# Kernel optimization log

Measured on AMD Instinct MI355X. Metric: run time of the kernel, lower is better.

Reference implementation:

```python
import jax, jax.numpy as jnp
import numpy as np

D_MODEL, N_STATE, L_MAX, BATCH = 256, 64, 2048, 16

def _to_c(x):
    return jax.lax.complex(x[..., 0], x[..., 1])

def setup_inputs() -> dict:
    key = jax.random.key(0)
    k_u, k_ct_r, k_ct_i, k_step = jax.random.split(key, 4)
    n, d = N_STATE, D_MODEL
    # --- HiPPO DPLR init (numpy, matches torch hippo_dplr) ---
    P = np.sqrt(1.0 + 2.0 * np.arange(1, n + 1, dtype=np.float64))
    A = np.tril(np.outer(P, P)) - np.diag(np.arange(1, n + 1, dtype=np.float64))
    A = -A
    p = 0.5 * np.sqrt(2.0 * np.arange(1, n + 1, dtype=np.float64) + 1.0)
    Ap = (A + np.outer(p, p)).astype(np.complex64)
    lam, V = np.linalg.eig(Ap)
    p_rot = V.conj().T @ p.astype(np.complex64)
    p_ri = np.stack([p_rot.real, p_rot.imag], -1).astype(np.float32)          # (n,2)
    lambda_ri = np.stack([lam.real, lam.imag], -1).astype(np.float32)         # (n,2)
    # --- B init: sqrt(2k+1), repeated over channels, zero imag ---
    B_r = np.sqrt(2.0 * np.arange(1, n + 1) + 1.0).astype(np.float32)
    B_ri = np.stack([np.tile(B_r, (d, 1)), np.zeros((d, n), np.float32)], -1) # (d,n,2)
    # --- Ct: xavier-normal complex ---
    std = float(np.sqrt(2.0 / (d + n)))
    Ct_r = jax.random.normal(k_ct_r, (d, n), jnp.float32) * (std / np.sqrt(2.0))
    Ct_i = jax.random.normal(k_ct_i, (d, n), jnp.float32) * (std / np.sqrt(2.0))
    Ct_ri = jnp.stack([Ct_r, Ct_i], -1)                                        # (d,n,2)
    Dp = jnp.ones((1, 1, d), jnp.float32)
    log_step = jax.random.uniform(k_step, (d,), jnp.float32) * (
        np.log(0.1) - np.log(0.001)) + np.log(0.001)
    u = jax.random.normal(k_u, (BATCH, L_MAX, d), jnp.float32)
    return {"u": u, "p_ri": jnp.asarray(p_ri), "lambda_ri": jnp.asarray(lambda_ri),
            "B_ri": jnp.asarray(B_ri), "Ct_ri": Ct_ri, "Dp": Dp, "log_step": log_step}

def reference(u, p_ri, lambda_ri, B_ri, Ct_ri, Dp, log_step):
    p = _to_c(p_ri)          # (n,)
    lam = _to_c(lambda_ri)   # (n,)
    B = _to_c(B_ri)          # (d,n)
    Ct = _to_c(Ct_ri)        # (d,n)
    L = u.shape[1]
    omega = jnp.exp(2j * jnp.pi * jnp.arange(L) / L).astype(jnp.complex64)  # (L,)
    step = jnp.exp(log_step)                                               # (d,)
    g = (2.0 / step)[:, None] * ((1.0 - omega) / (1.0 + omega))[None, :]   # (d,L)
    c = 2.0 / (1.0 + omega)                                                # (L,)
    inv = 1.0 / (g[:, :, None] - lam[None, None, :])                       # (d,L,n)
    k00 = jnp.einsum('dn,dln->dl', Ct.conj() * B, inv)
    k01 = jnp.einsum('dn,dln->dl', Ct.conj() * p[None, :], inv)
    k10 = jnp.einsum('dn,dln->dl', p.conj()[None, :] * B, inv)
    k11 = jnp.einsum('n,dln->dl', p.conj() * p, inv)
    at_roots = c[None, :] * (k00 - k01 * k10 / (1.0 + k11))                # (d,L)
    out = jnp.fft.ifft(at_roots, n=L, axis=-1)
    order = jnp.concatenate([jnp.zeros((1,), jnp.int32), jnp.arange(L - 1, 0, -1)])
    K = out[:, order].real[None]                                           # (1,d,L)
    # causal FFT convolution
    ud = jnp.fft.rfft(jnp.pad(u, ((0, 0), (0, L), (0, 0))), axis=1)        # (B,L+1,d)
    Kd = jnp.fft.rfft(jnp.pad(K, ((0, 0), (0, 0), (0, L))), axis=-1)       # (1,d,L+1)
    y = jnp.fft.irfft(jnp.transpose(ud, (0, 2, 1)) * Kd, axis=-1)[..., :L]
    y = jnp.transpose(y, (0, 2, 1)).astype(u.dtype)                        # (B,L,d)
    return y + Dp * u
```

## Files before the change

### kernel.cpp

```cpp
#include <hip/hip_runtime.h>
#include <math.h>

#define LLEN   2048
#define NFFT   4096
#define DMODEL 256
#define NSTATE 64
#define NBATCH 16
#define PI_F   3.14159265358979323846f

#define PADIDX(a) ((a) + ((a) >> 4))
#define LDSN  (NFFT + (NFFT >> 4))
#define LDSN2 (LLEN + (LLEN >> 4))
#define KSTRIDE 2056

__device__ inline float frcp(float x) { return __builtin_amdgcn_rcpf(x); }

#define RADIX4(ar0,ai0,ar1,ai1,ar2,ai2,ar3,ai3,S) do {                      \
    float s0r=(ar0)+(ar2), s0i=(ai0)+(ai2);                                 \
    float s1r=(ar0)-(ar2), s1i=(ai0)-(ai2);                                 \
    float s2r=(ar1)+(ar3), s2i=(ai1)+(ai3);                                 \
    float s3r=(ar1)-(ar3), s3i=(ai1)-(ai3);                                 \
    (ar0)=s0r+s2r; (ai0)=s0i+s2i;                                           \
    (ar2)=s0r-s2r; (ai2)=s0i-s2i;                                           \
    (ar1)=s1r-(S)*s3i; (ai1)=s1i+(S)*s3r;                                   \
    (ar3)=s1r+(S)*s3i; (ai3)=s1i-(S)*s3r;                                   \
} while (0)

template<int SIGN>
__device__ inline void dft16(float xr[16], float xi[16]) {
    const float S = (float)SIGN;
    const float C1 = 0.9238795325112867f, S1 = 0.3826834323650898f;
    const float C2 = 0.7071067811865476f;
    RADIX4(xr[0],xi[0], xr[4],xi[4], xr[8],xi[8],  xr[12],xi[12], S);
    RADIX4(xr[1],xi[1], xr[5],xi[5], xr[9],xi[9],  xr[13],xi[13], S);
    RADIX4(xr[2],xi[2], xr[6],xi[6], xr[10],xi[10],xr[14],xi[14], S);
    RADIX4(xr[3],xi[3], xr[7],xi[7], xr[11],xi[11],xr[15],xi[15], S);
#define TW(idx, wr_, wi_) { float tr = xr[idx]*(wr_) - xi[idx]*(wi_);       \
    xi[idx] = xr[idx]*(wi_) + xi[idx]*(wr_); xr[idx] = tr; }
    TW(5,  C1,  S*S1);
    TW(6,  C2,  S*C2);
    TW(7,  S1,  S*C1);
    TW(9,  C2,  S*C2);
    TW(10, 0.f, S);
    TW(11, -C2, S*C2);
    TW(13, S1,  S*C1);
    TW(14, -C2, S*C2);
    TW(15, -C1, -S*S1);
#undef TW
    RADIX4(xr[0],xi[0],  xr[1],xi[1],  xr[2],xi[2],  xr[3],xi[3],  S);
    RADIX4(xr[4],xi[4],  xr[5],xi[5],  xr[6],xi[6],  xr[7],xi[7],  S);
    RADIX4(xr[8],xi[8],  xr[9],xi[9],  xr[10],xi[10],xr[11],xi[11],S);
    RADIX4(xr[12],xi[12],xr[13],xi[13],xr[14],xi[14],xr[15],xi[15],S);
}

template<int SIGN>
__device__ inline void dft8(float xr[8], float xi[8]) {
    const float S = (float)SIGN;
    const float C2 = 0.7071067811865476f;
    RADIX4(xr[0],xi[0], xr[2],xi[2], xr[4],xi[4], xr[6],xi[6], S);
    RADIX4(xr[1],xi[1], xr[3],xi[3], xr[5],xi[5], xr[7],xi[7], S);
    { float tr = xr[3]*C2 - xi[3]*(S*C2); xi[3] = xr[3]*(S*C2) + xi[3]*C2; xr[3] = tr; }
    { float tr = -S*xi[5]; xi[5] = S*xr[5]; xr[5] = tr; }
    { float tr = xr[7]*(-C2) - xi[7]*(S*C2); xi[7] = xr[7]*(S*C2) + xi[7]*(-C2); xr[7] = tr; }
    float br[8], bi[8];
#pragma unroll
    for (int k = 0; k < 4; ++k) {
        br[k]   = xr[2*k] + xr[2*k+1]; bi[k]   = xi[2*k] + xi[2*k+1];
        br[k+4] = xr[2*k] - xr[2*k+1]; bi[k+4] = xi[2*k] - xi[2*k+1];
    }
#pragma unroll
    for (int k = 0; k < 8; ++k) { xr[k] = br[k]; xi[k] = bi[k]; }
}

template<int SIGN>
__device__ inline void tw_apply16(float xr[16], float xi[16], float ang) {
    float wr[16], wi[16];
    __sincosf(ang, &wi[1], &wr[1]);
#pragma unroll
    for (int k = 1; k < 8; ++k) {
        wr[2*k]   = wr[k]*wr[k] - wi[k]*wi[k];
        wi[2*k]   = 2.f * wr[k] * wi[k];
        wr[2*k+1] = wr[k]*wr[k+1] - wi[k]*wi[k+1];
        wi[2*k+1] = wr[k]*wi[k+1] + wi[k]*wr[k+1];
    }
#pragma unroll
    for (int t = 1; t < 16; ++t) {
        float tr = xr[t]*wr[t] - xi[t]*wi[t];
        xi[t] = xr[t]*wi[t] + xi[t]*wr[t];
        xr[t] = tr;
    }
}

template<int SIGN, int M, int L, bool PRUNE>
__device__ inline void stage16(float2* X, int j, bool active) {
    float xr[16], xi[16];
    const int p = j & (L - 1);
    if (active) {
#pragma unroll
        for (int t = 0; t < 16; ++t) {
            float2 v = X[PADIDX(j + t * M)];
            xr[t] = v.x; xi[t] = v.y;
        }
        tw_apply16<SIGN>(xr, xi, ((float)SIGN * 2.f * PI_F / (float)(16 * L)) * (float)p);
        dft16<SIGN>(xr, xi);
    }
    __syncthreads();
    if (active) {
        const int base = 16 * j - 15 * p;
#pragma unroll
        for (int k0 = 0; k0 < 4; ++k0)
#pragma unroll
            for (int k2 = 0; k2 < 4; ++k2) {
                const int u = k0 + 4 * k2;
                if (!PRUNE || u < 8) {
                    const int a = base + u * L;
                    X[PADIDX(a)] = make_float2(xr[4*k0+k2], xi[4*k0+k2]);
                }
            }
    }
    __syncthreads();
}

template<int SIGN, bool ZHI, bool PRUNE>
__device__ inline void fft4096_f2(float2* X, int tid) {
    float xr[16], xi[16];
#pragma unroll
    for (int t = 0; t < 16; ++t) {
        if (ZHI && t >= 8) { xr[t] = 0.f; xi[t] = 0.f; }
        else { float2 v = X[PADIDX(tid + t * 256)]; xr[t] = v.x; xi[t] = v.y; }
    }
    dft16<SIGN>(xr, xi);
    __syncthreads();
#pragma unroll
    for (int k0 = 0; k0 < 4; ++k0)
#pragma unroll
        for (int k2 = 0; k2 < 4; ++k2)
            X[PADIDX(16 * tid + k0 + 4 * k2)] = make_float2(xr[4*k0+k2], xi[4*k0+k2]);
    __syncthreads();
    stage16<SIGN, 256, 16,  false>(X, tid, true);
    stage16<SIGN, 256, 256, PRUNE>(X, tid, true);
}

template<int SIGN>
__device__ inline void fft2048_f2(float2* X, int tid) {
    float xr[8], xi[8];
#pragma unroll
    for (int t = 0; t < 8; ++t) {
        float2 v = X[PADIDX(tid + t * 256)];
        xr[t] = v.x; xi[t] = v.y;
    }
    dft8<SIGN>(xr, xi);
    __syncthreads();
#pragma unroll
    for (int u = 0; u < 8; ++u)
        X[PADIDX(8 * tid + u)] = make_float2(xr[u], xi[u]);
    __syncthreads();
    stage16<SIGN, 128, 8,   false>(X, tid, tid < 128);
    stage16<SIGN, 128, 128, false>(X, tid, tid < 128);
}

__global__ __launch_bounds__(256) void k_ar(const float* __restrict__ p_ri,
                                            const float* __restrict__ lambda_ri,
                                            const float* __restrict__ B_ri,
                                            const float* __restrict__ Ct_ri,
                                            const float* __restrict__ log_step,
                                            float2* __restrict__ ar_out) {
    __shared__ float4 c0[NSTATE], c1[NSTATE];
    __shared__ float2 lam[NSTATE];
    const int d = blockIdx.x >> 3;
    const int l = ((blockIdx.x & 7) << 8) | threadIdx.x;
    const int tid = threadIdx.x;
    if (tid < NSTATE) {
        const int n = tid;
        const float px = p_ri[2*n], py = p_ri[2*n+1];
        lam[n] = make_float2(lambda_ri[2*n], lambda_ri[2*n+1]);
        const float Bx = B_ri[(d*NSTATE+n)*2], By = B_ri[(d*NSTATE+n)*2+1];
        const float Cx = Ct_ri[(d*NSTATE+n)*2], Cy = Ct_ri[(d*NSTATE+n)*2+1];
        c0[n] = make_float4(Cx*Bx + Cy*By, Cx*By - Cy*Bx,
                            Cx*px + Cy*py, Cx*py - Cy*px);
        c1[n] = make_float4(px*Bx + py*By, px*By - py*Bx, px*px + py*py, 0.f);
    }
    __syncthreads();

    const float tos = 2.f * __expf(-log_step[d]);
    float sn, cs;
    sincosf(2.f * PI_F * (float)l / (float)LLEN, &sn, &cs);
    const float opx = 1.f + cs, opy = sn;
    const float omx = 1.f - cs, omy = -sn;
    const float inv_op = frcp(opx*opx + opy*opy);
    const float gx = tos * (omx*opx + omy*opy) * inv_op;
    const float gy = tos * (omy*opx - omx*opy) * inv_op;
    const float ccx = 2.f * opx * inv_op, ccy = -2.f * opy * inv_op;

    float k00x = 0, k00y = 0, k01x = 0, k01y = 0;
    float k10x = 0, k10y = 0, k11x = 0, k11y = 0;
    for (int n = 0; n < NSTATE; ++n) {
        const float2 lm = lam[n];
        const float dx = gx - lm.x, dy = gy - lm.y;
        const float idn = frcp(dx*dx + dy*dy);
        const float ix = dx * idn, iy = -dy * idn;
        const float4 a = c0[n];
        const float4 b = c1[n];
        k00x += a.x*ix - a.y*iy;  k00y += a.x*iy + a.y*ix;
        k01x += a.z*ix - a.w*iy;  k01y += a.z*iy + a.w*ix;
        k10x += b.x*ix - b.y*iy;  k10y += b.x*iy + b.y*ix;
        k11x += b.z*ix;           k11y += b.z*iy;
    }
    const float nx = k01x*k10x - k01y*k10y;
    const float ny = k01x*k10y + k01y*k10x;
    const float dpx = 1.f + k11x, dpy = k11y;
    const float idq = frcp(dpx*dpx + dpy*dpy);
    const float qx = (nx*dpx + ny*dpy) * idq;
    const float qy = (ny*dpx - nx*dpy) * idq;
    const float rx = k00x - qx, ry = k00y - qy;
    ar_out[(size_t)d * LLEN + l] = make_float2(ccx*rx - ccy*ry, ccx*ry + ccy*rx);
}

__global__ __launch_bounds__(256, 4) void k_mix(const float2* __restrict__ a_in,
                                                float2* __restrict__ Hc) {
    __shared__ float2 X[LDSN2];
    const int tid = threadIdx.x;
    const int d = blockIdx.x;
    const float isc = 1.f / (float)NFFT;
    const float4* a4 = (const float4*)(a_in + (size_t)d * LLEN);
#pragma unroll
    for (int k = 0; k < 4; ++k) {
        const int v = tid + k * 256;
        const float4 w = a4[v];
        X[PADIDX(2 * v)]     = make_float2(w.x, w.y);
        X[PADIDX(2 * v + 1)] = make_float2(w.z, w.w);
    }
    __syncthreads();

    float2* H = Hc + (size_t)d * KSTRIDE;
    for (int m = tid; m <= 1024; m += 256) {
        const float2 am = X[PADIDX(m)];
        const float2 an = X[PADIDX((LLEN - m) & (LLEN - 1))];
        H[2 * m] = make_float2((an.x + am.x) * 0.5f * isc,
                               (an.y - am.y) * 0.5f * isc);
    }
    fft2048_f2<-1>(X, tid);

#pragma unroll
    for (int k = 0; k < 8; ++k) {
        const int j = tid + k * 256;
        const int q = PADIDX(j);
        const float Kj = X[q].x * (1.f / (float)LLEN);
        float snj, csj;
        __sincosf(-PI_F * (float)j * (1.f / 2048.f), &snj, &csj);
        X[q] = make_float2(Kj * csj, Kj * snj);
    }
    __syncthreads();
    fft2048_f2<-1>(X, tid);

    for (int m = tid; m < 1024; m += 256) {
        const float2 w = X[PADIDX(m)];
        H[2 * m + 1] = make_float2(w.x * isc, w.y * isc);
    }
}

__global__ __launch_bounds__(256, 4) void k_fused(const float* __restrict__ u,
                                                  const float2* __restrict__ Hc,
                                                  const float* __restrict__ Dp,
                                                  float* __restrict__ out) {
    __shared__ float2 X[LDSN];
    const int i = blockIdx.x;
    const int x = i & 7;
    const int s = i >> 3;
    const int b  = s >> 4;
    const int cp = (x << 4) | (s & 15);
    const int ch = cp * 2;
    const int tid = threadIdx.x;

    const float* ub = u + (size_t)b * (LLEN * DMODEL) + ch;
    float2 uv[8];
#pragma unroll
    for (int k = 0; k < 8; ++k) {
        const int t = tid + k * 256;
        uv[k] = *(const float2*)(ub + (size_t)t * DMODEL);
        X[PADIDX(t)] = uv[k];
    }
    __syncthreads();
    fft4096_f2<-1, true, false>(X, tid);

    const float2* Ha = Hc + (size_t)ch * KSTRIDE;
    const float2* Hb = Ha + KSTRIDE;
    for (int f = tid; f <= NFFT / 2; f += 256) {
        const int fb = (NFFT - f) & (NFFT - 1);
        const float2 Za = X[PADIDX(f)], Zb = X[PADIDX(fb)];
        const float xax = 0.5f * (Za.x + Zb.x), xay = 0.5f * (Za.y - Zb.y);
        const float xbx = 0.5f * (Za.y + Zb.y), xby = -0.5f * (Za.x - Zb.x);
        const float2 A = Ha[f], B = Hb[f];
        const float yax = xax*A.x - xay*A.y, yay = xax*A.y + xay*A.x;
        const float ybx = xbx*B.x - xby*B.y, yby = xbx*B.y + xby*B.x;
        X[PADIDX(f)] = make_float2(yax - yby, yay + ybx);
        if (fb != f)
            X[PADIDX(fb)] = make_float2(yax + yby, ybx - yay);
    }
    __syncthreads();
    fft4096_f2<+1, false, true>(X, tid);

    const float2 dp = *(const float2*)(Dp + ch);
    float* ob = out + (size_t)b * (LLEN * DMODEL) + ch;
#pragma unroll
    for (int k = 0; k < 8; ++k) {
        const int t = tid + k * 256;
        const float2 v = X[PADIDX(t)];
        *(float2*)(ob + (size_t)t * DMODEL) =
            make_float2(v.x + dp.x * uv[k].x, v.y + dp.y * uv[k].y);
    }
}

extern "C" void kernel_launch(void* const* d_in, const int* in_sizes, int n_in,
                              void* d_out, int out_size, void* d_ws, size_t ws_size,
                              hipStream_t stream) {
    const float* u         = (const float*)d_in[0];
    const float* p_ri      = (const float*)d_in[1];
    const float* lambda_ri = (const float*)d_in[2];
    const float* B_ri      = (const float*)d_in[3];
    const float* Ct_ri     = (const float*)d_in[4];
    const float* Dp        = (const float*)d_in[5];
    const float* log_step  = (const float*)d_in[6];
    float* out = (float*)d_out;

    float2* Hc = (float2*)d_ws;
    float2* a  = (float2*)((char*)d_ws + (size_t)DMODEL * KSTRIDE * sizeof(float2));

    k_ar   <<<DMODEL * 8, 256, 0, stream>>>(p_ri, lambda_ri, B_ri, Ct_ri, log_step, a);
    k_mix  <<<DMODEL, 256, 0, stream>>>(a, Hc);
    k_fused<<<NBATCH * (DMODEL / 2), 256, 0, stream>>>(u, Hc, Dp, out);
}
```

Measured before the change: 179.4 us.

## Process four channels per block with float4 loads and batch four l per thread

The fused convolution kernel now has each block handle four channels. It loads u and stores out with float4 accesses instead of float2, and runs two sequential complex FFT passes through the same shared buffer, so global memory transactions are wider and there are half as many blocks. The resolvent kernel k_ar now computes four frequency points per thread, which amortizes the shared-memory reads of the per-state coefficients across them. The costs are more registers per thread, fewer blocks for latency hiding, and serialized FFT work within each block.

Measured after the change: 184.7 us. 2.9% more time.

```diff
diff --git a/kernel.cpp b/kernel.cpp
--- a/kernel.cpp
+++ b/kernel.cpp
@@ -167,8 +167,8 @@
                                             float2* __restrict__ ar_out) {
     __shared__ float4 c0[NSTATE], c1[NSTATE];
     __shared__ float2 lam[NSTATE];
-    const int d = blockIdx.x >> 3;
-    const int l = ((blockIdx.x & 7) << 8) | threadIdx.x;
+    const int d = blockIdx.x >> 1;
+    const int lbase = (blockIdx.x & 1) << 10;
     const int tid = threadIdx.x;
     if (tid < NSTATE) {
         const int n = tid;
@@ -183,37 +183,50 @@
     __syncthreads();
 
     const float tos = 2.f * __expf(-log_step[d]);
-    float sn, cs;
-    sincosf(2.f * PI_F * (float)l / (float)LLEN, &sn, &cs);
-    const float opx = 1.f + cs, opy = sn;
-    const float omx = 1.f - cs, omy = -sn;
-    const float inv_op = frcp(opx*opx + opy*opy);
-    const float gx = tos * (omx*opx + omy*opy) * inv_op;
-    const float gy = tos * (omy*opx - omx*opy) * inv_op;
-    const float ccx = 2.f * opx * inv_op, ccy = -2.f * opy * inv_op;
-
-    float k00x = 0, k00y = 0, k01x = 0, k01y = 0;
-    float k10x = 0, k10y = 0, k11x = 0, k11y = 0;
+    float gx[4], gy[4], ccx[4], ccy[4];
+    float k00x[4], k00y[4], k01x[4], k01y[4];
+    float k10x[4], k10y[4], k11x[4], k11y[4];
+#pragma unroll
+    for (int j = 0; j < 4; ++j) {
+        const int l = lbase + tid + (j << 8);
+        float sn, cs;
+        sincosf(2.f * PI_F * (float)l / (float)LLEN, &sn, &cs);
+        const float opx = 1.f + cs, opy = sn;
+        const float omx = 1.f - cs, omy = -sn;
+        const float inv_op = frcp(opx*opx + opy*opy);
+        gx[j] = tos * (omx*opx + omy*opy) * inv_op;
+        gy[j] = tos * (omy*opx - omx*opy) * inv_op;
+        ccx[j] = 2.f * opx * inv_op; ccy[j] = -2.f * opy * inv_op;
+        k00x[j]=0.f; k00y[j]=0.f; k01x[j]=0.f; k01y[j]=0.f;
+        k10x[j]=0.f; k10y[j]=0.f; k11x[j]=0.f; k11y[j]=0.f;
+    }
     for (int n = 0; n < NSTATE; ++n) {
         const float2 lm = lam[n];
-        const float dx = gx - lm.x, dy = gy - lm.y;
-        const float idn = frcp(dx*dx + dy*dy);
-        const float ix = dx * idn, iy = -dy * idn;
         const float4 a = c0[n];
         const float4 b = c1[n];
-        k00x += a.x*ix - a.y*iy;  k00y += a.x*iy + a.y*ix;
-        k01x += a.z*ix - a.w*iy;  k01y += a.z*iy + a.w*ix;
-        k10x += b.x*ix - b.y*iy;  k10y += b.x*iy + b.y*ix;
-        k11x += b.z*ix;           k11y += b.z*iy;
-    }
-    const float nx = k01x*k10x - k01y*k10y;
-    const float ny = k01x*k10y + k01y*k10x;
-    const float dpx = 1.f + k11x, dpy = k11y;
-    const float idq = frcp(dpx*dpx + dpy*dpy);
-    const float qx = (nx*dpx + ny*dpy) * idq;
-    const float qy = (ny*dpx - nx*dpy) * idq;
-    const float rx = k00x - qx, ry = k00y - qy;
-    ar_out[(size_t)d * LLEN + l] = make_float2(ccx*rx - ccy*ry, ccx*ry + ccy*rx);
+#pragma unroll
+        for (int j = 0; j < 4; ++j) {
+            const float dx = gx[j] - lm.x, dy = gy[j] - lm.y;
+            const float idn = frcp(dx*dx + dy*dy);
+            const float ix = dx * idn, iy = -dy * idn;
+            k00x[j] += a.x*ix - a.y*iy;  k00y[j] += a.x*iy + a.y*ix;
+            k01x[j] += a.z*ix - a.w*iy;  k01y[j] += a.z*iy + a.w*ix;
+            k10x[j] += b.x*ix - b.y*iy;  k10y[j] += b.x*iy + b.y*ix;
+            k11x[j] += b.z*ix;           k11y[j] += b.z*iy;
+        }
+    }
+#pragma unroll
+    for (int j = 0; j < 4; ++j) {
+        const float nx = k01x[j]*k10x[j] - k01y[j]*k10y[j];
+        const float ny = k01x[j]*k10y[j] + k01y[j]*k10x[j];
+        const float dpx = 1.f + k11x[j], dpy = k11y[j];
+        const float idq = frcp(dpx*dpx + dpy*dpy);
+        const float qx = (nx*dpx + ny*dpy) * idq;
+        const float qy = (ny*dpx - nx*dpy) * idq;
+        const float rx = k00x[j] - qx, ry = k00y[j] - qy;
+        ar_out[(size_t)d * LLEN + lbase + tid + (j << 8)] =
+            make_float2(ccx[j]*rx - ccy[j]*ry, ccx[j]*ry + ccy[j]*rx);
+    }
 }
 
 __global__ __launch_bounds__(256, 4) void k_mix(const float2* __restrict__ a_in,
@@ -259,32 +272,9 @@
     }
 }
 
-__global__ __launch_bounds__(256, 4) void k_fused(const float* __restrict__ u,
-                                                  const float2* __restrict__ Hc,
-                                                  const float* __restrict__ Dp,
-                                                  float* __restrict__ out) {
-    __shared__ float2 X[LDSN];
-    const int i = blockIdx.x;
-    const int x = i & 7;
-    const int s = i >> 3;
-    const int b  = s >> 4;
-    const int cp = (x << 4) | (s & 15);
-    const int ch = cp * 2;
-    const int tid = threadIdx.x;
-
-    const float* ub = u + (size_t)b * (LLEN * DMODEL) + ch;
-    float2 uv[8];
-#pragma unroll
-    for (int k = 0; k < 8; ++k) {
-        const int t = tid + k * 256;
-        uv[k] = *(const float2*)(ub + (size_t)t * DMODEL);
-        X[PADIDX(t)] = uv[k];
-    }
-    __syncthreads();
-    fft4096_f2<-1, true, false>(X, tid);
-
-    const float2* Ha = Hc + (size_t)ch * KSTRIDE;
-    const float2* Hb = Ha + KSTRIDE;
+__device__ inline void pointwise2(float2* __restrict__ X,
+                                  const float2* __restrict__ Ha,
+                                  const float2* __restrict__ Hb, int tid) {
     for (int f = tid; f <= NFFT / 2; f += 256) {
         const int fb = (NFFT - f) & (NFFT - 1);
         const float2 Za = X[PADIDX(f)], Zb = X[PADIDX(fb)];
@@ -298,16 +288,62 @@
             X[PADIDX(fb)] = make_float2(yax + yby, ybx - yay);
     }
     __syncthreads();
-    fft4096_f2<+1, false, true>(X, tid);
-
-    const float2 dp = *(const float2*)(Dp + ch);
-    float* ob = out + (size_t)b * (LLEN * DMODEL) + ch;
+}
+
+__global__ __launch_bounds__(256, 4) void k_fused(const float* __restrict__ u,
+                                                  const float2* __restrict__ Hc,
+                                                  const float* __restrict__ Dp,
+                                                  float* __restrict__ out) {
+    __shared__ float2 X[LDSN];
+    const int i = blockIdx.x;
+    const int x = i & 7;
+    const int s = i >> 3;
+    const int b = s >> 3;
+    const int q = (x << 3) | (s & 7);
+    const int ch = q * 4;
+    const int tid = threadIdx.x;
+
+    const float* ub = u + (size_t)b * (LLEN * DMODEL) + ch;
+    float2 uvA[8], zB[8];
 #pragma unroll
     for (int k = 0; k < 8; ++k) {
         const int t = tid + k * 256;
-        const float2 v = X[PADIDX(t)];
-        *(float2*)(ob + (size_t)t * DMODEL) =
-            make_float2(v.x + dp.x * uv[k].x, v.y + dp.y * uv[k].y);
+        const float4 v = *(const float4*)(ub + (size_t)t * DMODEL);
+        uvA[k] = make_float2(v.x, v.y);
+        zB[k]  = make_float2(v.z, v.w);
+        X[PADIDX(t)] = uvA[k];
+    }
+    __syncthreads();
+
+    fft4096_f2<-1, true, false>(X, tid);
+    pointwise2(X, Hc + (size_t)ch * KSTRIDE, Hc + (size_t)(ch + 1) * KSTRIDE, tid);
+    fft4096_f2<+1, false, true>(X, tid);
+
+    float2 yA[8];
+#pragma unroll
+    for (int k = 0; k < 8; ++k) {
+        const int t = tid + k * 256;
+        yA[k] = X[PADIDX(t)];
+        X[PADIDX(t)] = zB[k];
+    }
+    __syncthreads();
+
+    fft4096_f2<-1, true, false>(X, tid);
+    pointwise2(X, Hc + (size_t)(ch + 2) * KSTRIDE, Hc + (size_t)(ch + 3) * KSTRIDE, tid);
+    fft4096_f2<+1, false, true>(X, tid);
+
+    const float4 dp = *(const float4*)(Dp + ch);
+    float* ob = out + (size_t)b * (LLEN * DMODEL) + ch;
+#pragma unroll
+    for (int k = 0; k < 8; ++k) {
+        const int t = tid + k * 256;
+        const float2 yB = X[PADIDX(t)];
+        float4 o;
+        o.x = yA[k].x + dp.x * uvA[k].x;
+        o.y = yA[k].y + dp.y * uvA[k].y;
+        o.z = yB.x    + dp.z * zB[k].x;
+        o.w = yB.y    + dp.w * zB[k].y;
+        *(float4*)(ob + (size_t)t * DMODEL) = o;
     }
 }
 
@@ -326,7 +362,7 @@
     float2* Hc = (float2*)d_ws;
     float2* a  = (float2*)((char*)d_ws + (size_t)DMODEL * KSTRIDE * sizeof(float2));
 
-    k_ar   <<<DMODEL * 8, 256, 0, stream>>>(p_ri, lambda_ri, B_ri, Ct_ri, log_step, a);
+    k_ar   <<<DMODEL * 2, 256, 0, stream>>>(p_ri, lambda_ri, B_ri, Ct_ri, log_step, a);
     k_mix  <<<DMODEL, 256, 0, stream>>>(a, Hc);
-    k_fused<<<NBATCH * (DMODEL / 2), 256, 0, stream>>>(u, Hc, Dp, out);
-}
+    k_fused<<<NBATCH * (DMODEL / 4), 256, 0, stream>>>(u, Hc, Dp, out);
+}
```
